# Optimization experiments

Measured on AMD Instinct MI355X. Metric: run time of the kernel, lower is better.

Reference implementation:

```python
import jax, jax.numpy as jnp
import numpy as np

B, DIM, H, W = 8, 64, 64, 64
N_EMBED = 512
NNZ = 4          # num_nonzero OMP iterations
REG = 1e-7       # tiny Tikhonov term for the batched normal-equation solves


def batch_omp(X, D, S):
    """Batch OMP: for each signal pick S atoms greedily and solve LS on support.
    X: [N, d] signals, D: [d, K] dictionary with unit-norm atoms.
    Returns dense sparse code [N, K] with <= S nonzeros per row.
    Mathematically equivalent to the incremental-Cholesky Batch_OMP: at each
    step we solve G_II gamma = alpha0_I on the current support I.
    """
    N, K = X.shape[0], D.shape[1]
    G = D.T @ D                 # [K, K] Gram matrix (precomputed once)
    alpha0 = X @ D              # [N, K] initial correlations D^T x
    alpha = alpha0
    idx_cols = []
    gamma = None
    idx = None
    for k in range(S):          # static small loop over sparsity level
        j = jnp.argmax(jnp.abs(alpha), axis=1)                # [N] greedy atom
        idx_cols.append(j)
        idx = jnp.stack(idx_cols, axis=1)                     # [N, k+1]
        G_sub = G[idx[:, :, None], idx[:, None, :]]           # [N, k+1, k+1]
        rhs = jnp.take_along_axis(alpha0, idx, axis=1)        # [N, k+1]
        reg = REG * jnp.eye(k + 1, dtype=G.dtype)
        gamma = jnp.linalg.solve(G_sub + reg, rhs[..., None])[..., 0]  # [N, k+1]
        # residual correlations: alpha = alpha0 - G[:, I] gamma  (G symmetric)
        alpha = alpha0 - jnp.einsum('nak,na->nk', G[idx], gamma)
    code = jnp.zeros((N, K), X.dtype).at[jnp.arange(N)[:, None], idx].set(gamma)
    return code


def setup_inputs() -> dict:
    key = jax.random.key(0)
    kx, kd = jax.random.split(key)
    x = jax.random.normal(kx, (B, DIM, H, W), dtype=jnp.float32)
    dictionary = jax.random.normal(kd, (DIM, N_EMBED), dtype=jnp.float32)
    return {"x": x, "dictionary": dictionary}


def reference(x, dictionary):
    perm = jnp.transpose(x, (0, 2, 3, 1))            # [B, H, W, C]
    flat = perm.reshape(-1, DIM)                     # [N, C], N = B*H*W
    # normalize_dict=True: atoms normalized to unit L2 norm (in-place in torch)
    Dn = dictionary / jnp.linalg.norm(dictionary, axis=0, keepdims=True)
    code = batch_omp(flat, Dn, NNZ)                  # [N, K] (torch keeps [K, N])
    quant = (code @ Dn.T).reshape(perm.shape)        # reconstruction
    diff_enc = jnp.mean((quant - perm) ** 2)
    diff_dict = diff_enc                             # backward_dict=False branch
    # straight-through: perm + (quant - perm).detach() == quant in value
    out = jnp.transpose(quant, (0, 3, 1, 2))         # [B, C, H, W]
    ids = jnp.transpose(code.reshape(B, H, W, N_EMBED), (0, 3, 1, 2))  # [B, K, H, W]
    norm_0 = jnp.sum(code != 0, axis=1).astype(jnp.float32)  # L0 per signal, [N]
    num_steps = jnp.float32(NNZ)
    mean_D = jnp.mean(jnp.abs(Dn))
    mean_Z = jnp.mean(jnp.abs(code))
    norm_Z = jnp.mean(norm_0)
    topk_num = max(1, int(norm_0.shape[0] * 0.01))   # static: 327
    top_percentile = jnp.min(jax.lax.top_k(norm_0, topk_num)[0])
    num_zeros = jnp.sum(norm_0 == 0).astype(jnp.float32)
    return (out, diff_enc, diff_dict, ids, num_steps, mean_D, mean_Z,
            norm_Z, top_percentile, num_zeros)
```

## Files before the change

kernel.cpp:

```cpp
#include <hip/hip_runtime.h>
#include <cstdint>
#include <cstddef>

#define BQ 8
#define CDIM 64
#define HQ 64
#define WQ 64
#define KDIM 512
#define N_SIG 32768
#define S_NNZ 4

#define DIFF_ENC_OFF 2097152
#define DIFF_DICT_OFF 2097153
#define IDS_OFF 2097154
#define NUM_STEPS_OFF 18874370
#define MEAN_D_OFF 18874371
#define MEAN_Z_OFF 18874372
#define NORM_Z_OFF 18874373
#define TOP_PCT_OFF 18874374
#define NUM_ZEROS_OFF 18874375

#define WS_PD 16
#define WS_DNT 24
#define WS_G 32792
#define WS_WG 294936
#define WS_WI 426008

#define DNR_OFF 4194304

typedef float v2f __attribute__((ext_vector_type(2)));

__global__ __launch_bounds__(256) void k_g(const float* __restrict__ D,
                                           float* __restrict__ G,
                                           float* __restrict__ DnT,
                                           float* __restrict__ pd,
                                           float* __restrict__ Dnr,
                                           float* __restrict__ W) {
  __shared__ float Xs[64 * 64];
  __shared__ float Dns[64 * 64];
  __shared__ float partA[4][64];
  __shared__ float partB[4][64];
  __shared__ float invA[64];
  __shared__ float invB[64];
  int tid = threadIdx.x;
  int w = tid & 63, cq = tid >> 6;
  int ty = tid >> 4, tx = tid & 15;
  if (blockIdx.x == 0 && tid < 16) ((unsigned int*)W)[tid] = 0u;

  int ti = (int)blockIdx.x >> 3, tj = (int)blockIdx.x & 7;
#pragma unroll
  for (int p = 0; p < 16; ++p) {
    int c = p * 4 + cq;
    Xs[c * 64 + w] = D[(size_t)c * KDIM + ti * 64 + w];
    Dns[c * 64 + w] = D[(size_t)c * KDIM + tj * 64 + w];
  }
  __syncthreads();
  float ssA = 0.f, ssB = 0.f;
#pragma unroll
  for (int cc = 0; cc < 16; ++cc) {
    int c = cq * 16 + cc;
    float a = Xs[c * 64 + w];
    ssA = fmaf(a, a, ssA);
    float bv = Dns[c * 64 + w];
    ssB = fmaf(bv, bv, ssB);
  }
  partA[cq][w] = ssA;
  partB[cq][w] = ssB;
  __syncthreads();
  if (tid < 64) {
    invA[tid] = 1.0f / sqrtf(partA[0][tid] + partA[1][tid] + partA[2][tid] + partA[3][tid]);
    invB[tid] = 1.0f / sqrtf(partB[0][tid] + partB[1][tid] + partB[2][tid] + partB[3][tid]);
  }
  __syncthreads();
  if (ti == tj) {
    int kl = tid >> 2, cp = (tid & 3) * 16;
    float ia = invA[kl];
    int kg = ti * 64 + kl;
    float sabs = 0.f;
#pragma unroll
    for (int i = 0; i < 16; ++i) {
      int c = cp + i;
      float v = Xs[c * 64 + kl] * ia;
      DnT[(size_t)kg * CDIM + c] = v;
      Dnr[(size_t)c * KDIM + kg] = v;
      sabs += fabsf(v);
    }
#pragma unroll
    for (int off = 32; off >= 1; off >>= 1) sabs += __shfl_xor(sabs, off);
    __syncthreads();
    if ((tid & 63) == 0) partA[0][tid >> 6] = sabs;
    __syncthreads();
    if (tid == 0) pd[ti] = partA[0][0] + partA[0][1] + partA[0][2] + partA[0][3];
  }
  v2f acc[4][2] = {};
  for (int c = 0; c < 64; ++c) {
    float4 avv = *(const float4*)&Xs[c * 64 + ty * 4];
    float av[4] = {avv.x, avv.y, avv.z, avv.w};
    float4 bv = *(const float4*)&Dns[c * 64 + tx * 4];
    v2f b0 = {bv.x, bv.y}, b1 = {bv.z, bv.w};
#pragma unroll
    for (int i = 0; i < 4; ++i) {
      v2f a2 = {av[i], av[i]};
      acc[i][0] = __builtin_elementwise_fma(a2, b0, acc[i][0]);
      acc[i][1] = __builtin_elementwise_fma(a2, b1, acc[i][1]);
    }
  }
  float sn[4] = {invB[tx * 4], invB[tx * 4 + 1], invB[tx * 4 + 2], invB[tx * 4 + 3]};
#pragma unroll
  for (int i = 0; i < 4; ++i) {
    float im = invA[ty * 4 + i];
    float4 st = make_float4(acc[i][0].x * im * sn[0], acc[i][0].y * im * sn[1],
                            acc[i][1].x * im * sn[2], acc[i][1].y * im * sn[3]);
    *(float4*)&G[(size_t)(ti * 64 + ty * 4 + i) * KDIM + tj * 64 + tx * 4] = st;
  }
}

__device__ __forceinline__ float wave_absmax_u(float m) {
#define DPP_MAX(ctrl)                                                              \
  {                                                                                \
    int t_ = __builtin_amdgcn_update_dpp(0, __float_as_int(m), (ctrl), 0xf, 0xf,   \
                                         true);                                    \
    m = fmaxf(m, __int_as_float(t_));                                              \
  }
  DPP_MAX(0x111) DPP_MAX(0x112) DPP_MAX(0x114) DPP_MAX(0x118)
  DPP_MAX(0x142) DPP_MAX(0x143)
#undef DPP_MAX
  return __int_as_float(__builtin_amdgcn_readlane(__float_as_int(m), 63));
}

template <int SZ>
__device__ __forceinline__ void solve_sz(const float (&gs)[4][4], const float (&rhs)[4],
                                         float (&gamma)[4]) {
  float M[SZ][SZ];
  float y[SZ];
  float idg[SZ];
#pragma unroll
  for (int a = 0; a < SZ; ++a) {
    y[a] = rhs[a];
#pragma unroll
    for (int b = 0; b < SZ; ++b) M[a][b] = gs[a][b] + (a == b ? 1e-7f : 0.0f);
  }
#pragma unroll
  for (int p = 0; p < SZ; ++p) {
    float ip = __builtin_amdgcn_rcpf(M[p][p]);
    idg[p] = ip;
#pragma unroll
    for (int r = p + 1; r < SZ; ++r) {
      float f = M[r][p] * ip;
#pragma unroll
      for (int c = p + 1; c < SZ; ++c) M[r][c] = fmaf(-f, M[p][c], M[r][c]);
      y[r] = fmaf(-f, y[p], y[r]);
    }
  }
#pragma unroll
  for (int r = SZ - 1; r >= 0; --r) {
    float t = y[r];
#pragma unroll
    for (int c = r + 1; c < SZ; ++c) t = fmaf(-M[r][c], gamma[c], t);
    gamma[r] = t * idg[r];
  }
}

template <int K>
__device__ __forceinline__ void omp_step3(int lane, const float* __restrict__ G,
                                          const float* as_row,
                                          float (&al)[8], float (&Grow)[3][8],
                                          float (&gs)[4][4], float (&rhs)[4],
                                          int (&idx)[4], float (&gamma)[4]) {
  float mx0 = fabsf(al[0]);
  int mi = 0;
#pragma unroll
  for (int m = 1; m < 8; ++m) {
    float v = fabsf(al[m]);
    mi = (v > mx0) ? m : mi;
    mx0 = fmaxf(v, mx0);
  }
  float mx = wave_absmax_u(mx0);
  unsigned long long bm = __ballot(mx0 == mx);
  int wl = (int)__builtin_ctzll(bm);
  int mwin = __builtin_amdgcn_readlane(mi, wl);
  int sk = wl * 8 + mwin;
  idx[K] = sk;

  const float* grow_base = G + (size_t)sk * KDIM;
  float4 p0, p1;
  if constexpr (K < 3) {
    p0 = *(const float4*)&as_row[lane * 8];
    p1 = *(const float4*)&as_row[lane * 8 + 4];
  }
  if constexpr (K < 3) {
    const float4* gp = (const float4*)(grow_base + lane * 8);
    float4 r0 = gp[0], r1 = gp[1];
    Grow[K][0] = r0.x; Grow[K][1] = r0.y; Grow[K][2] = r0.z; Grow[K][3] = r0.w;
    Grow[K][4] = r1.x; Grow[K][5] = r1.y; Grow[K][6] = r1.z; Grow[K][7] = r1.w;
  }

#pragma unroll
  for (int b2 = 0; b2 < K; ++b2) {
    float v = grow_base[idx[b2]];
    gs[K][b2] = v;
    gs[b2][K] = v;
  }
  gs[K][K] = grow_base[sk];
  rhs[K] = as_row[sk];

  solve_sz<K + 1>(gs, rhs, gamma);

  if constexpr (K < 3) {
    float a0v[8] = {p0.x, p0.y, p0.z, p0.w, p1.x, p1.y, p1.z, p1.w};
#pragma unroll
    for (int m = 0; m < 8; ++m) {
      float acc2 = a0v[m];
#pragma unroll
      for (int a = 0; a <= K; ++a) acc2 = fmaf(-gamma[a], Grow[a][m], acc2);
      al[m] = acc2;
    }
  }
}

__global__ __launch_bounds__(256, 8) void k_fused(const float* __restrict__ X,
                                                  const float* __restrict__ Dnr,
                                                  const float* __restrict__ G,
                                                  float4* __restrict__ wg,
                                                  int4* __restrict__ wi) {
  __shared__ __align__(16) float AS[8 * 512];
  int tid = threadIdx.x;
  int lane = tid & 63;
  int wv = __builtin_amdgcn_readfirstlane(tid >> 6);
  int bid = (int)blockIdx.x;
  int bh = bid >> 3, w0 = (bid & 7) * 8;
  int b = bh >> 6, h = bh & 63;

  v2f acc[8] = {};
  const v2f* dp = (const v2f*)Dnr + wv * 64 + lane;
  const float* xbase = X + ((size_t)b * CDIM * HQ + h) * WQ + w0;
#pragma unroll 4
  for (int c = 0; c < 64; ++c) {
    v2f d = dp[c * 256];
    const float4* xp = (const float4*)(xbase + (size_t)c * (HQ * WQ));
    float4 x0 = xp[0], x1 = xp[1];
    float xv[8] = {x0.x, x0.y, x0.z, x0.w, x1.x, x1.y, x1.z, x1.w};
#pragma unroll
    for (int s = 0; s < 8; ++s) {
      v2f xx = {xv[s], xv[s]};
      acc[s] = __builtin_elementwise_fma(xx, d, acc[s]);
    }
  }

#pragma unroll
  for (int s = 0; s < 8; ++s)
    *(v2f*)&AS[s * 512 + wv * 128 + lane * 2] = acc[s];
  __syncthreads();

#pragma unroll 1
  for (int s = 0; s < 2; ++s) {
    int sb = wv * 2 + s;
    int n = bid * 8 + sb;
    const float* as_row = &AS[sb * 512];
    float4 q0 = *(const float4*)&as_row[lane * 8];
    float4 q1 = *(const float4*)&as_row[lane * 8 + 4];
    float al[8] = {q0.x, q0.y, q0.z, q0.w, q1.x, q1.y, q1.z, q1.w};
    float Grow[3][8];
    float gs[4][4];
    float rhs[4];
    int idx[4];
    float gamma[4];
    omp_step3<0>(lane, G, as_row, al, Grow, gs, rhs, idx, gamma);
    omp_step3<1>(lane, G, as_row, al, Grow, gs, rhs, idx, gamma);
    omp_step3<2>(lane, G, as_row, al, Grow, gs, rhs, idx, gamma);
    omp_step3<3>(lane, G, as_row, al, Grow, gs, rhs, idx, gamma);
    bool k0 = (idx[0] != idx[1]) && (idx[0] != idx[2]) && (idx[0] != idx[3]);
    bool k1 = (idx[1] != idx[2]) && (idx[1] != idx[3]);
    bool k2 = (idx[2] != idx[3]);
    if (lane == 0) {
      wg[n] = make_float4(k0 ? gamma[0] : 0.f, k1 ? gamma[1] : 0.f,
                          k2 ? gamma[2] : 0.f, gamma[3]);
      wi[n] = make_int4(idx[0], idx[1], idx[2], idx[3]);
    }
  }
}

__global__ __launch_bounds__(256) void k_ei(const float* __restrict__ X,
                                            const float* __restrict__ DnT,
                                            const float4* __restrict__ wg,
                                            const int4* __restrict__ wi,
                                            float* __restrict__ out,
                                            double* __restrict__ accs,
                                            int* __restrict__ hist) {
  __shared__ __align__(16) int sIdx[64][4];
  __shared__ __align__(16) float sKg[64][4];
  __shared__ float q[64 * 65];
  __shared__ float red[4];
  int tid = threadIdx.x;

  if (blockIdx.x < 512) {
    int bh = blockIdx.x;
    int b = bh >> 6, h = bh & 63;
    if (tid < 64) {
      int w = tid;
      int n = bh * 64 + w;
      int4 iv = wi[n];
      float4 gv = wg[n];
      sIdx[w][0] = iv.x; sIdx[w][1] = iv.y; sIdx[w][2] = iv.z; sIdx[w][3] = iv.w;
      sKg[w][0] = gv.x; sKg[w][1] = gv.y; sKg[w][2] = gv.z; sKg[w][3] = gv.w;
      int nz = (int)(gv.x != 0.f) + (int)(gv.y != 0.f) +
               (int)(gv.z != 0.f) + (int)(gv.w != 0.f);
      float s = fabsf(gv.x) + fabsf(gv.y) + fabsf(gv.z) + fabsf(gv.w);
#pragma unroll
      for (int off = 32; off >= 1; off >>= 1) s += __shfl_xor(s, off);
#pragma unroll
      for (int v = 0; v < 5; ++v) {
        unsigned long long m = __ballot(nz == v);
        if (tid == 0) {
          int c = (int)__popcll(m);
          if (c) atomicAdd(&hist[v], c);
        }
      }
      if (tid == 0) atomicAdd(&accs[0], (double)s);
    }
    __syncthreads();

    int w2 = tid & 63, p = tid >> 6, c0 = p * 16;
    float acc[16] = {};
#pragma unroll
    for (int s = 0; s < 4; ++s) {
      int ks = sIdx[w2][s];
      float g = sKg[w2][s];
      const float4* dp = (const float4*)(DnT + (size_t)ks * CDIM + c0);
#pragma unroll
      for (int i4 = 0; i4 < 4; ++i4) {
        float4 d = dp[i4];
        acc[i4 * 4 + 0] = fmaf(g, d.x, acc[i4 * 4 + 0]);
        acc[i4 * 4 + 1] = fmaf(g, d.y, acc[i4 * 4 + 1]);
        acc[i4 * 4 + 2] = fmaf(g, d.z, acc[i4 * 4 + 2]);
        acc[i4 * 4 + 3] = fmaf(g, d.w, acc[i4 * 4 + 3]);
      }
    }
#pragma unroll
    for (int i = 0; i < 16; ++i) q[(c0 + i) * 65 + w2] = acc[i];
    __syncthreads();

    float sumsq = 0.f;
#pragma unroll
    for (int pass = 0; pass < 16; ++pass) {
      int c = pass * 4 + p;
      float qv = q[c * 65 + w2];
      size_t off = (((size_t)b * CDIM + c) * HQ + h) * WQ + w2;
      float xv = X[off];
      float d = qv - xv;
      sumsq = fmaf(d, d, sumsq);
      out[off] = qv;
    }

#pragma unroll
    for (int off = 32; off >= 1; off >>= 1) sumsq += __shfl_xor(sumsq, off);
    if ((tid & 63) == 0) red[tid >> 6] = sumsq;
    __syncthreads();
    if (tid == 0) atomicAdd(&accs[1], (double)(red[0] + red[1] + red[2] + red[3]));
  } else {
    int bid = blockIdx.x - 512;
    int bh = bid >> 2, kq = bid & 3;
    int b = bh >> 6, h = bh & 63;
    if (tid < 64) {
      int n = bh * 64 + tid;
      *(int4*)&sIdx[tid][0] = wi[n];
      *(float4*)&sKg[tid][0] = wg[n];
    }
    __syncthreads();
    int w4 = (tid & 15) * 4, kl = tid >> 4;
    int4 I0 = *(const int4*)&sIdx[w4][0];
    int4 I1 = *(const int4*)&sIdx[w4 + 1][0];
    int4 I2 = *(const int4*)&sIdx[w4 + 2][0];
    int4 I3 = *(const int4*)&sIdx[w4 + 3][0];
    float4 G0 = *(const float4*)&sKg[w4][0];
    float4 G1 = *(const float4*)&sKg[w4 + 1][0];
    float4 G2 = *(const float4*)&sKg[w4 + 2][0];
    float4 G3 = *(const float4*)&sKg[w4 + 3][0];
    float* ids = out + IDS_OFF;
    size_t base = (((size_t)b * KDIM + kq * 128 + kl) * HQ + h) * WQ + w4;
#pragma unroll
    for (int pass = 0; pass < 8; ++pass) {
      int k = kq * 128 + pass * 16 + kl;
      float4 v;
      v.x = (k == I0.w) ? G0.w : (k == I0.z) ? G0.z : (k == I0.y) ? G0.y : (k == I0.x) ? G0.x : 0.f;
      v.y = (k == I1.w) ? G1.w : (k == I1.z) ? G1.z : (k == I1.y) ? G1.y : (k == I1.x) ? G1.x : 0.f;
      v.z = (k == I2.w) ? G2.w : (k == I2.z) ? G2.z : (k == I2.y) ? G2.y : (k == I2.x) ? G2.x : 0.f;
      v.w = (k == I3.w) ? G3.w : (k == I3.z) ? G3.z : (k == I3.y) ? G3.y : (k == I3.x) ? G3.x : 0.f;
      *(float4*)&ids[base + (size_t)pass * 16 * 4096] = v;
    }
  }
}

__global__ __launch_bounds__(64) void k_final(const double* __restrict__ accs,
                                              const int* __restrict__ hist,
                                              const float* __restrict__ pd,
                                              float* __restrict__ out) {
  if (threadIdx.x == 0) {
    float sumAbsD = 0.f;
#pragma unroll
    for (int i = 0; i < 8; ++i) sumAbsD += pd[i];
    double sumAbsZ = accs[0], sumSq = accs[1];
    float diff = (float)(sumSq / 2097152.0);
    out[DIFF_ENC_OFF] = diff;
    out[DIFF_DICT_OFF] = diff;
    out[NUM_STEPS_OFF] = 4.0f;
    out[MEAN_D_OFF] = sumAbsD / 32768.0f;
    out[MEAN_Z_OFF] = (float)(sumAbsZ / 16777216.0);
    int h0 = hist[0], h1 = hist[1], h2 = hist[2], h3 = hist[3], h4 = hist[4];
    out[NORM_Z_OFF] = (float)((double)(h1 + 2 * h2 + 3 * h3 + 4 * h4) / 32768.0);
    int cum = 0, res = 0;
    for (int v = 4; v >= 0; --v) {
      cum += hist[v];
      if (cum >= 327) { res = v; break; }
    }
    out[TOP_PCT_OFF] = (float)res;
    out[NUM_ZEROS_OFF] = (float)h0;
  }
}

extern "C" void kernel_launch(void* const* d_in, const int* in_sizes, int n_in,
                              void* d_out, int out_size, void* d_ws, size_t ws_size,
                              hipStream_t stream) {
  (void)in_sizes; (void)n_in; (void)out_size; (void)ws_size;
  const float* X = (const float*)d_in[0];
  const float* D = (const float*)d_in[1];
  float* out = (float*)d_out;
  float* W = (float*)d_ws;
  double* accs = (double*)d_ws;
  int* hist = (int*)W + 4;
  float* pd = W + WS_PD;
  float* DnT = W + WS_DNT;
  float* G = W + WS_G;
  float4* wgam = (float4*)(W + WS_WG);
  int4* widx = (int4*)(W + WS_WI);
  float* Dnr = out + DNR_OFF;

  hipLaunchKernelGGL(k_g, dim3(64), dim3(256), 0, stream, D, G, DnT, pd, Dnr, W);
  hipLaunchKernelGGL(k_fused, dim3(4096), dim3(256), 0, stream, X, Dnr, G, wgam, widx);
  hipLaunchKernelGGL(k_ei, dim3(2560), dim3(256), 0, stream, X, DnT, wgam, widx, out, accs, hist);
  hipLaunchKernelGGL(k_final, dim3(1), dim3(64), 0, stream, accs, hist, pd, out);
}
```

Baseline: 165.1 us.

## Process two signals per wavefront with half-wave OMP and swizzled LDS

The OMP phase now maps one signal to each 32-lane half of a wavefront, with 16 correlations per lane, instead of running two signals sequentially across the full wave. The argmax uses a shortened DPP reduction that yields per-half maxima. LDS addresses are XOR-swizzled to avoid bank conflicts on the 64-byte-stride reads. Occupancy hints change from launch_bounds(256,8) to waves_per_eu(2,4), and the wider per-lane arrays raise register pressure.

```diff
diff --git a/kernel.cpp b/kernel.cpp
--- a/kernel.cpp
+++ b/kernel.cpp
@@ -27,6 +27,8 @@
 #define WS_WI 426008
 
 #define DNR_OFF 4194304
+
+#define SWZ(a) ((a) ^ ((((a) >> 5) & 7) << 2))
 
 typedef float v2f __attribute__((ext_vector_type(2)));
 
@@ -115,17 +117,17 @@
   }
 }
 
-__device__ __forceinline__ float wave_absmax_u(float m) {
+__device__ __forceinline__ void half_absmax(float m, float& mxA, float& mxB) {
 #define DPP_MAX(ctrl)                                                              \
   {                                                                                \
     int t_ = __builtin_amdgcn_update_dpp(0, __float_as_int(m), (ctrl), 0xf, 0xf,   \
                                          true);                                    \
     m = fmaxf(m, __int_as_float(t_));                                              \
   }
-  DPP_MAX(0x111) DPP_MAX(0x112) DPP_MAX(0x114) DPP_MAX(0x118)
-  DPP_MAX(0x142) DPP_MAX(0x143)
+  DPP_MAX(0x111) DPP_MAX(0x112) DPP_MAX(0x114) DPP_MAX(0x118) DPP_MAX(0x142)
 #undef DPP_MAX
-  return __int_as_float(__builtin_amdgcn_readlane(__float_as_int(m), 63));
+  mxA = __int_as_float(__builtin_amdgcn_readlane(__float_as_int(m), 31));
+  mxB = __int_as_float(__builtin_amdgcn_readlane(__float_as_int(m), 63));
 }
 
 template <int SZ>
@@ -162,55 +164,62 @@
 }
 
 template <int K>
-__device__ __forceinline__ void omp_step3(int lane, const float* __restrict__ G,
-                                          const float* as_row,
-                                          float (&al)[8], float (&Grow)[3][8],
-                                          float (&gs)[4][4], float (&rhs)[4],
-                                          int (&idx)[4], float (&gamma)[4]) {
-  float mx0 = fabsf(al[0]);
-  int mi = 0;
-#pragma unroll
-  for (int m = 1; m < 8; ++m) {
-    float v = fabsf(al[m]);
-    mi = (v > mx0) ? m : mi;
-    mx0 = fmaxf(v, mx0);
-  }
-  float mx = wave_absmax_u(mx0);
-  unsigned long long bm = __ballot(mx0 == mx);
-  int wl = (int)__builtin_ctzll(bm);
-  int mwin = __builtin_amdgcn_readlane(mi, wl);
-  int sk = wl * 8 + mwin;
+__device__ __forceinline__ void omp_half(int l5, int hh, const float* __restrict__ G,
+                                         const float* as_row,
+                                         const float (&a08)[16], float (&al)[16],
+                                         float (&Grow)[3][16], float (&gs)[4][4],
+                                         float (&rhs)[4], int (&idx)[4],
+                                         float (&gamma)[4]) {
+  float v[16];
+#pragma unroll
+  for (int m = 0; m < 16; ++m) v[m] = fabsf(al[m]);
+  float m01 = fmaxf(v[0], v[1]),   m23 = fmaxf(v[2], v[3]);
+  float m45 = fmaxf(v[4], v[5]),   m67 = fmaxf(v[6], v[7]);
+  float m89 = fmaxf(v[8], v[9]),   mAB = fmaxf(v[10], v[11]);
+  float mCD = fmaxf(v[12], v[13]), mEF = fmaxf(v[14], v[15]);
+  float mx0 = fmaxf(fmaxf(fmaxf(m01, m23), fmaxf(m45, m67)),
+                    fmaxf(fmaxf(m89, mAB), fmaxf(mCD, mEF)));
+  int mi = 15;
+#pragma unroll
+  for (int m = 14; m >= 0; --m) mi = (v[m] == mx0) ? m : mi;
+  float mxA, mxB;
+  half_absmax(mx0, mxA, mxB);
+  float mxh = hh ? mxB : mxA;
+  unsigned long long bm = __ballot(mx0 == mxh);
+  unsigned bmA = (unsigned)bm;
+  unsigned bmB = (unsigned)(bm >> 32);
+  int wlA = (int)__builtin_ctz(bmA);
+  int wlB = (int)__builtin_ctz(bmB);
+  int skA = wlA * 16 + __builtin_amdgcn_readlane(mi, wlA);
+  int skB = wlB * 16 + __builtin_amdgcn_readlane(mi, 32 + wlB);
+  int sk = hh ? skB : skA;
   idx[K] = sk;
 
-  const float* grow_base = G + (size_t)sk * KDIM;
-  float4 p0, p1;
+  rhs[K] = as_row[SWZ(sk)];
+
+  const float* gb = G + (size_t)sk * KDIM;
   if constexpr (K < 3) {
-    p0 = *(const float4*)&as_row[lane * 8];
-    p1 = *(const float4*)&as_row[lane * 8 + 4];
-  }
+#pragma unroll
+    for (int jj = 0; jj < 4; ++jj) {
+      float4 r = *(const float4*)&gb[l5 * 16 + jj * 4];
+      Grow[K][jj * 4 + 0] = r.x; Grow[K][jj * 4 + 1] = r.y;
+      Grow[K][jj * 4 + 2] = r.z; Grow[K][jj * 4 + 3] = r.w;
+    }
+  }
+#pragma unroll
+  for (int b2 = 0; b2 < K; ++b2) {
+    float vv = gb[idx[b2]];
+    gs[K][b2] = vv;
+    gs[b2][K] = vv;
+  }
+  gs[K][K] = gb[sk];
+
+  solve_sz<K + 1>(gs, rhs, gamma);
+
   if constexpr (K < 3) {
-    const float4* gp = (const float4*)(grow_base + lane * 8);
-    float4 r0 = gp[0], r1 = gp[1];
-    Grow[K][0] = r0.x; Grow[K][1] = r0.y; Grow[K][2] = r0.z; Grow[K][3] = r0.w;
-    Grow[K][4] = r1.x; Grow[K][5] = r1.y; Grow[K][6] = r1.z; Grow[K][7] = r1.w;
-  }
-
-#pragma unroll
-  for (int b2 = 0; b2 < K; ++b2) {
-    float v = grow_base[idx[b2]];
-    gs[K][b2] = v;
-    gs[b2][K] = v;
-  }
-  gs[K][K] = grow_base[sk];
-  rhs[K] = as_row[sk];
-
-  solve_sz<K + 1>(gs, rhs, gamma);
-
-  if constexpr (K < 3) {
-    float a0v[8] = {p0.x, p0.y, p0.z, p0.w, p1.x, p1.y, p1.z, p1.w};
-#pragma unroll
-    for (int m = 0; m < 8; ++m) {
-      float acc2 = a0v[m];
+#pragma unroll
+    for (int m = 0; m < 16; ++m) {
+      float acc2 = a08[m];
 #pragma unroll
       for (int a = 0; a <= K; ++a) acc2 = fmaf(-gamma[a], Grow[a][m], acc2);
       al[m] = acc2;
@@ -218,11 +227,13 @@
   }
 }
 
-__global__ __launch_bounds__(256, 8) void k_fused(const float* __restrict__ X,
-                                                  const float* __restrict__ Dnr,
-                                                  const float* __restrict__ G,
-                                                  float4* __restrict__ wg,
-                                                  int4* __restrict__ wi) {
+__global__ __launch_bounds__(256)
+__attribute__((amdgpu_waves_per_eu(2, 4)))
+void k_fused(const float* __restrict__ X,
+             const float* __restrict__ Dnr,
+             const float* __restrict__ G,
+             float4* __restrict__ wg,
+             int4* __restrict__ wi) {
   __shared__ __align__(16) float AS[8 * 512];
   int tid = threadIdx.x;
   int lane = tid & 63;
@@ -247,36 +258,44 @@
     }
   }
 
+  int as_w = SWZ(wv * 128 + lane * 2);
 #pragma unroll
   for (int s = 0; s < 8; ++s)
-    *(v2f*)&AS[s * 512 + wv * 128 + lane * 2] = acc[s];
+    *(v2f*)&AS[s * 512 + as_w] = acc[s];
   __syncthreads();
 
-#pragma unroll 1
-  for (int s = 0; s < 2; ++s) {
-    int sb = wv * 2 + s;
-    int n = bid * 8 + sb;
-    const float* as_row = &AS[sb * 512];
-    float4 q0 = *(const float4*)&as_row[lane * 8];
-    float4 q1 = *(const float4*)&as_row[lane * 8 + 4];
-    float al[8] = {q0.x, q0.y, q0.z, q0.w, q1.x, q1.y, q1.z, q1.w};
-    float Grow[3][8];
-    float gs[4][4];
-    float rhs[4];
-    int idx[4];
-    float gamma[4];
-    omp_step3<0>(lane, G, as_row, al, Grow, gs, rhs, idx, gamma);
-    omp_step3<1>(lane, G, as_row, al, Grow, gs, rhs, idx, gamma);
-    omp_step3<2>(lane, G, as_row, al, Grow, gs, rhs, idx, gamma);
-    omp_step3<3>(lane, G, as_row, al, Grow, gs, rhs, idx, gamma);
-    bool k0 = (idx[0] != idx[1]) && (idx[0] != idx[2]) && (idx[0] != idx[3]);
-    bool k1 = (idx[1] != idx[2]) && (idx[1] != idx[3]);
-    bool k2 = (idx[2] != idx[3]);
-    if (lane == 0) {
-      wg[n] = make_float4(k0 ? gamma[0] : 0.f, k1 ? gamma[1] : 0.f,
-                          k2 ? gamma[2] : 0.f, gamma[3]);
-      wi[n] = make_int4(idx[0], idx[1], idx[2], idx[3]);
-    }
+  int hh = lane >> 5;
+  int l5 = lane & 31;
+  int sig = wv * 2 + hh;
+  const float* as_row = &AS[sig * 512];
+  float a08[16];
+#pragma unroll
+  for (int jj = 0; jj < 4; ++jj) {
+    int f0 = l5 * 16 + jj * 4;
+    float4 q = *(const float4*)&as_row[SWZ(f0)];
+    a08[jj * 4 + 0] = q.x; a08[jj * 4 + 1] = q.y;
+    a08[jj * 4 + 2] = q.z; a08[jj * 4 + 3] = q.w;
+  }
+  float al[16];
+#pragma unroll
+  for (int m = 0; m < 16; ++m) al[m] = a08[m];
+  float Grow[3][16];
+  float gs[4][4];
+  float rhs[4];
+  int idx[4];
+  float gamma[4];
+  omp_half<0>(l5, hh, G, as_row, a08, al, Grow, gs, rhs, idx, gamma);
+  omp_half<1>(l5, hh, G, as_row, a08, al, Grow, gs, rhs, idx, gamma);
+  omp_half<2>(l5, hh, G, as_row, a08, al, Grow, gs, rhs, idx, gamma);
+  omp_half<3>(l5, hh, G, as_row, a08, al, Grow, gs, rhs, idx, gamma);
+  bool k0 = (idx[0] != idx[1]) && (idx[0] != idx[2]) && (idx[0] != idx[3]);
+  bool k1 = (idx[1] != idx[2]) && (idx[1] != idx[3]);
+  bool k2 = (idx[2] != idx[3]);
+  if ((lane & 31) == 0) {
+    int n = bid * 8 + sig;
+    wg[n] = make_float4(k0 ? gamma[0] : 0.f, k1 ? gamma[1] : 0.f,
+                        k2 ? gamma[2] : 0.f, gamma[3]);
+    wi[n] = make_int4(idx[0], idx[1], idx[2], idx[3]);
   }
 }
 
```

Measured after the change: 168.7 us. 2.1% more time.
